# Optimization experiments

Hardware: AMD Instinct MI355X
Metric: run time of the kernel (lower is better)

## Reference

```python
import jax, jax.numpy as jnp
import numpy as np

B, T, D, H = 2, 2048, 1024, 16
HD = D // H            # head dim = 64
WINDOW = 512           # sliding-window size
EPS = 1e-6
ROPE_BASE = 10000.0


def setup_inputs() -> dict:
    key = jax.random.key(0)
    ks = jax.random.split(key, 5)
    s = 0.02  # init scale for dense kernels
    return {
        "x": jax.random.normal(ks[0], (B, T, D), jnp.float32),
        "Wq": jax.random.normal(ks[1], (D, D), jnp.float32) * s,
        "Wk": jax.random.normal(ks[2], (D, D), jnp.float32) * s,
        "Wv": jax.random.normal(ks[3], (D, D), jnp.float32) * s,
        "Wo": jax.random.normal(ks[4], (D, D), jnp.float32) * s,
        "q_scale": jnp.ones((HD,), jnp.float32),
        "k_scale": jnp.ones((HD,), jnp.float32),
        "sink_logit": jnp.zeros((H,), jnp.float32),
    }


def _rmsnorm(x, scale):
    # x: [..., HD]
    var = jnp.mean(jnp.square(x), axis=-1, keepdims=True)
    return x * jax.lax.rsqrt(var + EPS) * scale


def _rope(x):
    # x: [B, H, T, HD]; standard rotate-half RoPE over the full head dim
    half = HD // 2
    inv_freq = 1.0 / (ROPE_BASE ** (jnp.arange(0, HD, 2, dtype=jnp.float32) / HD))  # [half]
    t = jnp.arange(T, dtype=jnp.float32)
    freqs = t[:, None] * inv_freq[None, :]                # [T, half]
    emb = jnp.concatenate([freqs, freqs], axis=-1)        # [T, HD]
    cos = jnp.cos(emb)[None, None]                        # [1,1,T,HD]
    sin = jnp.sin(emb)[None, None]
    x1, x2 = x[..., :half], x[..., half:]
    rot = jnp.concatenate([-x2, x1], axis=-1)
    return x * cos + rot * sin


def reference(x, Wq, Wk, Wv, Wo, q_scale, k_scale, sink_logit):
    # projections -> [B, T, H, HD]
    q = (x @ Wq).reshape(B, T, H, HD)
    k = (x @ Wk).reshape(B, T, H, HD)
    v = (x @ Wv).reshape(B, T, H, HD)
    # QK RMSNorm over head dim
    q = _rmsnorm(q, q_scale)
    k = _rmsnorm(k, k_scale)
    # -> [B, H, T, HD], then RoPE
    q = _rope(q.transpose(0, 2, 1, 3))
    k = _rope(k.transpose(0, 2, 1, 3))
    v = v.transpose(0, 2, 1, 3)
    # causal sliding-window mask
    idx = jnp.arange(T)
    rel = idx[None, :] - idx[:, None]                     # key - query
    mask = ((rel <= 0) & (rel > -WINDOW))[None, None]     # [1,1,T,T]
    scale = HD ** (-0.5)
    scores = jnp.einsum('bhtd,bhsd->bhts', q, k) * scale
    scores = jnp.where(mask, scores, -jnp.inf)
    # sink-augmented softmax: append per-head sink logit to denominator
    sink = jnp.broadcast_to(sink_logit.reshape(1, H, 1, 1), (B, H, T, 1))
    aug = jnp.concatenate([scores.astype(jnp.float32), sink.astype(jnp.float32)], axis=-1)
    weights = jax.nn.softmax(aug, axis=-1)[..., :T].astype(scores.dtype)
    out = jnp.einsum('bhts,bhsd->bhtd', weights, v)
    out = out.transpose(0, 2, 1, 3).reshape(B, T, D)
    return out @ Wo
```

## Files before the change

### kernel.cpp

```cpp
#include <hip/hip_runtime.h>
#include <math.h>

#define CB 2
#define CT 2048
#define CD 1024
#define CH 16
#define CHD 64
#define CWINDOW 512

typedef __bf16 bf16x8 __attribute__((ext_vector_type(8)));
typedef float floatx4 __attribute__((ext_vector_type(4)));

__device__ __forceinline__ unsigned short f2bf(float f) {
  union { float f; unsigned int u; } v;
  v.f = f;
  unsigned int u = v.u;
  u += 0x7fffu + ((u >> 16) & 1u);
  return (unsigned short)(u >> 16);
}
__device__ __forceinline__ unsigned short f2bf_trunc(float f) {
  union { float f; unsigned int u; } v;
  v.f = f;
  return (unsigned short)(v.u >> 16);
}
__device__ __forceinline__ float bf2f(unsigned int h) {
  union { unsigned int u; float f; } v;
  v.u = h << 16;
  return v.f;
}

__global__ __launch_bounds__(256) void cvt_all(const float* __restrict__ x,
                                               const float* __restrict__ Wq,
                                               const float* __restrict__ Wk,
                                               const float* __restrict__ Wv,
                                               const float* __restrict__ Wo,
                                               unsigned short* __restrict__ xb,
                                               unsigned short* __restrict__ WqT,
                                               unsigned short* __restrict__ WkT,
                                               unsigned short* __restrict__ WvT,
                                               unsigned short* __restrict__ WoT) {
  const int z = blockIdx.z;
  if (z < 4) {
    const float* W = z == 0 ? Wq : z == 1 ? Wk : z == 2 ? Wv : Wo;
    unsigned short* Wt = z == 0 ? WqT : z == 1 ? WkT : z == 2 ? WvT : WoT;
    __shared__ float tile[64][65];
    const int k0 = blockIdx.x * 64, n0 = blockIdx.y * 64;
    const int c = threadIdx.x & 63, r4 = threadIdx.x >> 6;
#pragma unroll
    for (int i = 0; i < 16; ++i) {
      int r = i * 4 + r4;
      tile[r][c] = W[(size_t)(k0 + r) * CD + n0 + c];
    }
    __syncthreads();
#pragma unroll
    for (int i = 0; i < 16; ++i) {
      int r = i * 4 + r4;
      Wt[(size_t)(n0 + r) * CD + k0 + c] = f2bf(tile[c][r]);
    }
  } else {
    const int idx = (z - 4) * 256 + blockIdx.y * 16 + blockIdx.x;
    const int i = idx * 256 + threadIdx.x;
    float4 a = ((const float4*)x)[i * 2];
    float4 b = ((const float4*)x)[i * 2 + 1];
    uint4 o;
    o.x = (unsigned int)f2bf(a.x) | ((unsigned int)f2bf(a.y) << 16);
    o.y = (unsigned int)f2bf(a.z) | ((unsigned int)f2bf(a.w) << 16);
    o.z = (unsigned int)f2bf(b.x) | ((unsigned int)f2bf(b.y) << 16);
    o.w = (unsigned int)f2bf(b.z) | ((unsigned int)f2bf(b.w) << 16);
    ((uint4*)xb)[i] = o;
  }
}

__device__ __forceinline__ void async16(const unsigned short* g, unsigned short* l) {
  __builtin_amdgcn_global_load_lds(
      (const __attribute__((address_space(1))) unsigned int*)g,
      (__attribute__((address_space(3))) unsigned int*)l, 16, 0, 0);
}

__device__ __forceinline__ bf16x8 frag64(const unsigned short* base, int row, int ks, int lane) {
  const int phys = (((ks << 2) + (lane >> 4)) ^ (lane & 7)) << 3;
  return *(const bf16x8*)&base[(row << 6) + phys];
}

template <int MODE, int BM>
__device__ __forceinline__ void mfma_gemm_body(const unsigned short* __restrict__ A,
                                               const unsigned short* __restrict__ Bt,
                                               void* __restrict__ Cout,
                                               const float* __restrict__ scale,
                                               float oscale, int m0, int n0,
                                               unsigned short* __restrict__ As,
                                               unsigned short* __restrict__ Bs) {
  constexpr int K = CD;
  constexpr int MT = BM / 32;
  const int tid = threadIdx.x;
  const int wave = tid >> 6, lane = tid & 63;
  const int mq = (wave & 1) * (BM / 2), nq = (wave >> 1) * 64;

  floatx4 acc[MT][4] = {};
  const int l7 = lane & 7, l8 = lane >> 3;
  const int sxc = (l7 ^ l8) * 8;
  const int fr = lane & 15;

  for (int k0 = 0; k0 < K; k0 += 64) {
    __syncthreads();
#pragma unroll
    for (int it = 0; it < BM / 32; ++it) {
      const int s = wave * (BM / 32) + it;
      async16(A + (size_t)(m0 + s * 8 + l8) * K + k0 + sxc, &As[s * 512]);
    }
#pragma unroll
    for (int it = 0; it < 4; ++it) {
      const int s = wave * 4 + it;
      async16(Bt + (size_t)(n0 + s * 8 + l8) * K + k0 + sxc, &Bs[s * 512]);
    }
    __syncthreads();
#pragma unroll
    for (int ks = 0; ks < 2; ++ks) {
      bf16x8 af[MT], bg[4];
#pragma unroll
      for (int mt = 0; mt < MT; ++mt)
        af[mt] = frag64(As, mq + mt * 16 + fr, ks, lane);
#pragma unroll
      for (int nt = 0; nt < 4; ++nt)
        bg[nt] = frag64(Bs, nq + nt * 16 + fr, ks, lane);
#pragma unroll
      for (int mt = 0; mt < MT; ++mt)
#pragma unroll
        for (int nt = 0; nt < 4; ++nt)
          acc[mt][nt] = __builtin_amdgcn_mfma_f32_16x16x32_bf16(af[mt], bg[nt], acc[mt][nt], 0, 0, 0);
    }
  }

  if (MODE == 1) {
    const int c = lane & 15;
    const int g = lane >> 4;
    const int hh = (n0 + nq) >> 6;
    const float kf = -0.2878231366242557f;
    const float inv0 = __expf((float)c * kf);
    const float inv1 = __expf((float)(16 + c) * kf);
    float sc[4];
#pragma unroll
    for (int nt = 0; nt < 4; ++nt) sc[nt] = scale[nt * 16 + c];
#pragma unroll
    for (int mt = 0; mt < MT; ++mt) {
#pragma unroll
      for (int i = 0; i < 4; ++i) {
        const int m = m0 + mq + mt * 16 + g * 4 + i;
        const int b = m >> 11, t = m & (CT - 1);
        float v0 = acc[mt][0][i], v1 = acc[mt][1][i];
        float v2 = acc[mt][2][i], v3 = acc[mt][3][i];
        float ss = v0 * v0 + v1 * v1 + v2 * v2 + v3 * v3;
#pragma unroll
        for (int off = 8; off > 0; off >>= 1) ss += __shfl_xor(ss, off);
        const float rs = rsqrtf(ss * (1.0f / 64.0f) + 1e-6f);
        v0 *= rs * sc[0];
        v1 *= rs * sc[1];
        v2 *= rs * sc[2];
        v3 *= rs * sc[3];
        const float tf = (float)t;
        const float a0 = tf * inv0, a1 = tf * inv1;
        const float s0 = __sinf(a0), c0 = __cosf(a0);
        const float s1 = __sinf(a1), c1 = __cosf(a1);
        unsigned short* dst = (unsigned short*)Cout + ((size_t)(b * CH + hh) * CT + t) * CHD;
        ushort4 o;
        o.x = f2bf((v0 * c0 - v2 * s0) * oscale);
        o.y = f2bf((v1 * c1 - v3 * s1) * oscale);
        o.z = f2bf((v2 * c0 + v0 * s0) * oscale);
        o.w = f2bf((v3 * c1 + v1 * s1) * oscale);
        *(ushort4*)&dst[4 * c] = o;
      }
    }
  } else {
#pragma unroll
    for (int mt = 0; mt < MT; ++mt) {
#pragma unroll
      for (int nt = 0; nt < 4; ++nt) {
        const int col = n0 + nq + nt * 16 + (lane & 15);
        if (MODE == 2) {
          const int mb = m0 + mq + mt * 16 + (lane >> 4) * 4;
          const int b = mb >> 11, t = mb & (CT - 1);
          const int h = col >> 6, d = col & 63;
          ushort4 o;
          o.x = f2bf(acc[mt][nt][0]);
          o.y = f2bf(acc[mt][nt][1]);
          o.z = f2bf(acc[mt][nt][2]);
          o.w = f2bf(acc[mt][nt][3]);
          *(ushort4*)&((unsigned short*)Cout)[((size_t)(b * CH + h) * CHD + d) * CT + t] = o;
        } else {
#pragma unroll
          for (int i = 0; i < 4; ++i) {
            const int m = m0 + mq + mt * 16 + (lane >> 4) * 4 + i;
            ((float*)Cout)[(size_t)m * CD + col] = acc[mt][nt][i];
          }
        }
      }
    }
  }
}

__global__ __launch_bounds__(256, 3) void gemm_qkv_mfma(const unsigned short* __restrict__ xb,
                                                        const unsigned short* __restrict__ WqT,
                                                        const unsigned short* __restrict__ WkT,
                                                        const unsigned short* __restrict__ WvT,
                                                        unsigned short* __restrict__ Qh,
                                                        unsigned short* __restrict__ Kh,
                                                        unsigned short* __restrict__ Vt,
                                                        const float* __restrict__ q_scale,
                                                        const float* __restrict__ k_scale) {
  __shared__ unsigned short As[128 * 64];
  __shared__ unsigned short Bs[128 * 64];
  const unsigned int L = blockIdx.x + 32u * blockIdx.y + 256u * blockIdx.z;
  const unsigned int x = L & 7u;
  const unsigned int j = L >> 3;
  const unsigned int gm = x & 3u;
  const unsigned int gw = x >> 2;
  const unsigned int jm = j & 7u;
  const unsigned int jp = j >> 3;
  const int m0 = (int)(gm * 8u + jm) * 128;
  const unsigned int vp = gw * 12u + jp;
  const int n0 = (int)(vp & 7u) * 128;
  const int bz = (int)(vp >> 3);
  if (bz == 2) {
    mfma_gemm_body<2, 128>(xb, WvT, Vt, nullptr, 1.0f, m0, n0, As, Bs);
  } else if (bz == 0) {
    mfma_gemm_body<1, 128>(xb, WqT, Qh, q_scale, 0.125f, m0, n0, As, Bs);
  } else {
    mfma_gemm_body<1, 128>(xb, WkT, Kh, k_scale, 1.0f, m0, n0, As, Bs);
  }
}

__global__ __launch_bounds__(256, 3) void gemm_out_mfma(const unsigned short* __restrict__ AO,
                                                        const unsigned short* __restrict__ WoT,
                                                        float* __restrict__ out) {
  __shared__ unsigned short As[64 * 64];
  __shared__ unsigned short Bs[128 * 64];
  const unsigned int L = blockIdx.x + 64u * blockIdx.y;
  const unsigned int x = L & 7u;
  const unsigned int j = L >> 3;
  const unsigned int jm = j & 7u;
  const unsigned int jp = j >> 3;
  const int m0 = (int)(x * 8u + jm) * 64;
  const int n0 = (int)jp * 128;
  mfma_gemm_body<0, 64>(AO, WoT, out, nullptr, 1.0f, m0, n0, As, Bs);
}

__global__ __launch_bounds__(256, 2) void attn_mfma(const unsigned short* __restrict__ Qh,
                                                    const unsigned short* __restrict__ Kh,
                                                    const unsigned short* __restrict__ Vt,
                                                    const float* __restrict__ sink_logit,
                                                    unsigned short* __restrict__ AO) {
  __shared__ unsigned short Qs[128 * 64];
  __shared__ unsigned short Ks[2][64 * 64];
  __shared__ unsigned short Vs[2][64 * 64];
  __shared__ unsigned short Ps[128 * 72];

  const int tid = threadIdx.x;
  const int w = tid >> 6, lane = tid & 63;
  const unsigned int L = blockIdx.x + 16u * blockIdx.y;
  const int qb = (int)((L >> 3) & 15u);
  const int bh = (int)(L & 7u) * 4 + (int)(L >> 7);
  const int b = bh >> 4, h = bh & 15;
  const int q0 = qb * 128;
  const unsigned short* Qb = Qh + (size_t)bh * CT * CHD;
  const unsigned short* Kb = Kh + (size_t)bh * CT * CHD;
  const unsigned short* Vb = Vt + (size_t)bh * CHD * CT;

  const int l7 = lane & 7, l8 = lane >> 3;
  const int sx8 = (l7 ^ l8) * 8;

  const int kb_lo = (qb >= 4) ? (qb * 2 - 8) : 0;
  const int kb_hi = qb * 2 + 1;

#pragma unroll
  for (int s = 0; s < 4; ++s) {
    const int slab = w * 4 + s;
    async16(Qb + (size_t)(q0 + slab * 8 + l8) * CHD + sx8, &Qs[slab * 512]);
  }
#pragma unroll
  for (int s = 0; s < 2; ++s) {
    const int slab = w * 2 + s;
    const int row = slab * 8 + l8;
    async16(Kb + (size_t)(kb_lo * 64 + row) * CHD + sx8, &Ks[0][slab * 512]);
    async16(Vb + (size_t)row * CT + kb_lo * 64 + sx8, &Vs[0][slab * 512]);
  }
  __syncthreads();

  bf16x8 qf[2][2];
#pragma unroll
  for (int nt = 0; nt < 2; ++nt)
#pragma unroll
    for (int ks = 0; ks < 2; ++ks)
      qf[nt][ks] = frag64(Qs, w * 32 + nt * 16 + (lane & 15), ks, lane);

  bf16x8 vones;
#pragma unroll
  for (int i = 0; i < 8; ++i) vones[i] = (__bf16)1.0f;

  floatx4 acc[4][2] = {};
  floatx4 lsacc[2] = {};
  const int qw = q0 + w * 32;

  int cur = 0;
  for (int kb = kb_lo; kb <= kb_hi; ++kb) {
    if (kb < kb_hi) {
#pragma unroll
      for (int s = 0; s < 2; ++s) {
        const int slab = w * 2 + s;
        const int row = slab * 8 + l8;
        async16(Kb + (size_t)((kb + 1) * 64 + row) * CHD + sx8, &Ks[cur ^ 1][slab * 512]);
        async16(Vb + (size_t)row * CT + (kb + 1) * 64 + sx8, &Vs[cur ^ 1][slab * 512]);
      }
    }

    const int kmin = kb * 64, kmax = kb * 64 + 63;
    if (!(kmin > qw + 31 || kmax <= qw - CWINDOW)) {
      const unsigned short* Kc = Ks[cur];
      const unsigned short* Vc = Vs[cur];

      floatx4 st[4][2] = {};
#pragma unroll
      for (int ks = 0; ks < 2; ++ks) {
        bf16x8 kf[4];
#pragma unroll
        for (int mt = 0; mt < 4; ++mt)
          kf[mt] = frag64(Kc, mt * 16 + (lane & 15), ks, lane);
        __builtin_amdgcn_s_setprio(1);
#pragma unroll
        for (int mt = 0; mt < 4; ++mt)
#pragma unroll
          for (int nt = 0; nt < 2; ++nt)
            st[mt][nt] = __builtin_amdgcn_mfma_f32_16x16x32_bf16(kf[mt], qf[nt][ks], st[mt][nt], 0, 0, 0);
        __builtin_amdgcn_s_setprio(0);
      }

      const bool need_c = (kmax > qw);
      const bool need_w = (kmin <= qw + 31 - CWINDOW);
#pragma unroll
      for (int mt = 0; mt < 4; ++mt) {
#pragma unroll
        for (int nt = 0; nt < 2; ++nt) {
          const int s_base = kb * 64 + mt * 16 + (lane >> 4) * 4;
          const int t_g = q0 + w * 32 + nt * 16 + (lane & 15);
          ushort4 pk;
#pragma unroll
          for (int i = 0; i < 4; ++i) {
            float sv = st[mt][nt][i];
            if (need_c || need_w) {
              const int s_g = s_base + i;
              const bool ok = (!need_c || (s_g <= t_g)) && (!need_w || (s_g > t_g - CWINDOW));
              sv = ok ? sv : -INFINITY;
            }
            ((unsigned short*)&pk)[i] = f2bf_trunc(__expf(sv));
          }
          const int qrow = w * 32 + nt * 16 + (lane & 15);
          const int scol = mt * 16 + (lane >> 4) * 4;
          *(ushort4*)&Ps[qrow * 72 + scol] = pk;
        }
      }

#pragma unroll
      for (int ks = 0; ks < 2; ++ks) {
        bf16x8 vf[4], pf[2];
#pragma unroll
        for (int mt = 0; mt < 4; ++mt)
          vf[mt] = frag64(Vc, mt * 16 + (lane & 15), ks, lane);
#pragma unroll
        for (int nt = 0; nt < 2; ++nt) {
          const int qrow = w * 32 + nt * 16 + (lane & 15);
          pf[nt] = *(const bf16x8*)&Ps[qrow * 72 + ks * 32 + (lane >> 4) * 8];
        }
        __builtin_amdgcn_s_setprio(1);
#pragma unroll
        for (int mt = 0; mt < 4; ++mt)
#pragma unroll
          for (int nt = 0; nt < 2; ++nt)
            acc[mt][nt] = __builtin_amdgcn_mfma_f32_16x16x32_bf16(vf[mt], pf[nt], acc[mt][nt], 0, 0, 0);
#pragma unroll
        for (int nt = 0; nt < 2; ++nt)
          lsacc[nt] = __builtin_amdgcn_mfma_f32_16x16x32_bf16(vones, pf[nt], lsacc[nt], 0, 0, 0);
        __builtin_amdgcn_s_setprio(0);
      }
    }

    asm volatile("s_waitcnt vmcnt(0)" ::: "memory");
    __builtin_amdgcn_s_barrier();
    cur ^= 1;
  }

  const float sinkw = __expf(sink_logit[h]);
  float inv[2];
#pragma unroll
  for (int nt = 0; nt < 2; ++nt) inv[nt] = 1.0f / (lsacc[nt][0] + sinkw);
#pragma unroll
  for (int mt = 0; mt < 4; ++mt) {
#pragma unroll
    for (int nt = 0; nt < 2; ++nt) {
      const int t_g = q0 + w * 32 + nt * 16 + (lane & 15);
      const int d0 = mt * 16 + (lane >> 4) * 4;
      ushort4 o;
      o.x = f2bf(acc[mt][nt][0] * inv[nt]);
      o.y = f2bf(acc[mt][nt][1] * inv[nt]);
      o.z = f2bf(acc[mt][nt][2] * inv[nt]);
      o.w = f2bf(acc[mt][nt][3] * inv[nt]);
      *(ushort4*)&AO[(size_t)(b * CT + t_g) * CD + h * CHD + d0] = o;
    }
  }
}

extern "C" void kernel_launch(void* const* d_in, const int* in_sizes, int n_in,
                              void* d_out, int out_size, void* d_ws, size_t ws_size,
                              hipStream_t stream) {
  (void)in_sizes;
  (void)n_in;
  (void)out_size;
  (void)ws_size;
  const float* x = (const float*)d_in[0];
  const float* Wq = (const float*)d_in[1];
  const float* Wk = (const float*)d_in[2];
  const float* Wv = (const float*)d_in[3];
  const float* Wo = (const float*)d_in[4];
  const float* q_scale = (const float*)d_in[5];
  const float* k_scale = (const float*)d_in[6];
  const float* sink = (const float*)d_in[7];
  float* out = (float*)d_out;

  const size_t per = (size_t)CB * CH * CT * CHD;
  unsigned short* Qh = (unsigned short*)d_ws;
  unsigned short* Kh = Qh + per;
  unsigned short* Vt = Kh + per;
  unsigned short* AO = Vt + per;
  unsigned short* xb = AO + per;
  unsigned short* WqT = xb + per;
  unsigned short* WkT = WqT + (size_t)CD * CD;
  unsigned short* WvT = WkT + (size_t)CD * CD;
  unsigned short* WoT = WvT + (size_t)CD * CD;

  dim3 blk(256);
  cvt_all<<<dim3(16, 16, 12), blk, 0, stream>>>(x, Wq, Wk, Wv, Wo, xb, WqT, WkT, WvT, WoT);
  gemm_qkv_mfma<<<dim3(32, 8, 3), blk, 0, stream>>>(xb, WqT, WkT, WvT, Qh, Kh, Vt, q_scale, k_scale);
  attn_mfma<<<dim3(CT / 128, CB * CH), blk, 0, stream>>>(Qh, Kh, Vt, sink, AO);
  gemm_out_mfma<<<dim3(64, 8), blk, 0, stream>>>(AO, WoT, out);
}
```

Baseline: 156.6 us.

## Triple-buffer GEMM K-tiles with async LDS loads and a single barrier per step

```diff
diff --git a/kernel.cpp b/kernel.cpp
--- a/kernel.cpp
+++ b/kernel.cpp
@@ -77,9 +77,49 @@
       (__attribute__((address_space(3))) unsigned int*)l, 16, 0, 0);
 }
 
-__device__ __forceinline__ bf16x8 frag64(const unsigned short* base, int row, int ks, int lane) {
-  const int phys = (((ks << 2) + (lane >> 4)) ^ (lane & 7)) << 3;
-  return *(const bf16x8*)&base[(row << 6) + phys];
+__device__ __forceinline__ bf16x8 frag32(const unsigned short* base, int row, int lane) {
+  const int phys = ((lane >> 4) ^ (row & 3)) << 3;
+  return *(const bf16x8*)&base[(row << 5) + phys];
+}
+
+template <int BM>
+__device__ __forceinline__ void gemm_stage(const unsigned short* __restrict__ A,
+                                           const unsigned short* __restrict__ Bt,
+                                           unsigned short* __restrict__ As_s,
+                                           unsigned short* __restrict__ Bs_s,
+                                           int m0, int n0, int t, int wave, int lane) {
+  const int row_in = lane >> 2;
+  const int src_c = ((lane & 3) ^ (row_in & 3)) * 8;
+  const int k0 = t * 32;
+#pragma unroll
+  for (int it = 0; it < BM / 64; ++it) {
+    const int sub = wave * (BM / 64) + it;
+    async16(A + (size_t)(m0 + sub * 16 + row_in) * CD + k0 + src_c, &As_s[sub * 512]);
+  }
+#pragma unroll
+  for (int it = 0; it < 2; ++it) {
+    const int sub = wave * 2 + it;
+    async16(Bt + (size_t)(n0 + sub * 16 + row_in) * CD + k0 + src_c, &Bs_s[sub * 512]);
+  }
+}
+
+template <int MT>
+__device__ __forceinline__ void gemm_compute(const unsigned short* __restrict__ As_s,
+                                             const unsigned short* __restrict__ Bs_s,
+                                             floatx4 (&acc)[MT][4], int mq, int nq, int lane) {
+  const int fr = lane & 15;
+  bf16x8 af[MT], bg[4];
+#pragma unroll
+  for (int mt = 0; mt < MT; ++mt) af[mt] = frag32(As_s, mq + mt * 16 + fr, lane);
+#pragma unroll
+  for (int nt = 0; nt < 4; ++nt) bg[nt] = frag32(Bs_s, nq + nt * 16 + fr, lane);
+  __builtin_amdgcn_s_setprio(1);
+#pragma unroll
+  for (int mt = 0; mt < MT; ++mt)
+#pragma unroll
+    for (int nt = 0; nt < 4; ++nt)
+      acc[mt][nt] = __builtin_amdgcn_mfma_f32_16x16x32_bf16(af[mt], bg[nt], acc[mt][nt], 0, 0, 0);
+  __builtin_amdgcn_s_setprio(0);
 }
 
 template <int MODE, int BM>
@@ -90,46 +130,39 @@
                                                float oscale, int m0, int n0,
                                                unsigned short* __restrict__ As,
                                                unsigned short* __restrict__ Bs) {
-  constexpr int K = CD;
+  constexpr int NT = CD / 32;
   constexpr int MT = BM / 32;
+  constexpr int ASLOT = BM * 32;
+  constexpr int BSLOT = 128 * 32;
   const int tid = threadIdx.x;
   const int wave = tid >> 6, lane = tid & 63;
   const int mq = (wave & 1) * (BM / 2), nq = (wave >> 1) * 64;
 
   floatx4 acc[MT][4] = {};
-  const int l7 = lane & 7, l8 = lane >> 3;
-  const int sxc = (l7 ^ l8) * 8;
-  const int fr = lane & 15;
-
-  for (int k0 = 0; k0 < K; k0 += 64) {
-    __syncthreads();
-#pragma unroll
-    for (int it = 0; it < BM / 32; ++it) {
-      const int s = wave * (BM / 32) + it;
-      async16(A + (size_t)(m0 + s * 8 + l8) * K + k0 + sxc, &As[s * 512]);
-    }
-#pragma unroll
-    for (int it = 0; it < 4; ++it) {
-      const int s = wave * 4 + it;
-      async16(Bt + (size_t)(n0 + s * 8 + l8) * K + k0 + sxc, &Bs[s * 512]);
-    }
-    __syncthreads();
-#pragma unroll
-    for (int ks = 0; ks < 2; ++ks) {
-      bf16x8 af[MT], bg[4];
-#pragma unroll
-      for (int mt = 0; mt < MT; ++mt)
-        af[mt] = frag64(As, mq + mt * 16 + fr, ks, lane);
-#pragma unroll
-      for (int nt = 0; nt < 4; ++nt)
-        bg[nt] = frag64(Bs, nq + nt * 16 + fr, ks, lane);
-#pragma unroll
-      for (int mt = 0; mt < MT; ++mt)
-#pragma unroll
-        for (int nt = 0; nt < 4; ++nt)
-          acc[mt][nt] = __builtin_amdgcn_mfma_f32_16x16x32_bf16(af[mt], bg[nt], acc[mt][nt], 0, 0, 0);
-    }
-  }
+
+  gemm_stage<BM>(A, Bt, As, Bs, m0, n0, 0, wave, lane);
+  gemm_stage<BM>(A, Bt, As + ASLOT, Bs + BSLOT, m0, n0, 1, wave, lane);
+  if constexpr (BM == 128) asm volatile("s_waitcnt vmcnt(4)" ::: "memory");
+  else asm volatile("s_waitcnt vmcnt(3)" ::: "memory");
+  __builtin_amdgcn_s_barrier();
+
+#pragma unroll 1
+  for (int j = 0; j < (NT - 2) / 3; ++j) {
+#pragma unroll
+    for (int u = 0; u < 3; ++u) {
+      const int t = j * 3 + u;
+      const int ss = (u + 2) % 3;
+      gemm_stage<BM>(A, Bt, As + ss * ASLOT, Bs + ss * BSLOT, m0, n0, t + 2, wave, lane);
+      gemm_compute<MT>(As + u * ASLOT, Bs + u * BSLOT, acc, mq, nq, lane);
+      if constexpr (BM == 128) asm volatile("s_waitcnt vmcnt(4)" ::: "memory");
+      else asm volatile("s_waitcnt vmcnt(3)" ::: "memory");
+      __builtin_amdgcn_s_barrier();
+    }
+  }
+  gemm_compute<MT>(As + 0 * ASLOT, Bs + 0 * BSLOT, acc, mq, nq, lane);
+  asm volatile("s_waitcnt vmcnt(0)" ::: "memory");
+  __builtin_amdgcn_s_barrier();
+  gemm_compute<MT>(As + 1 * ASLOT, Bs + 1 * BSLOT, acc, mq, nq, lane);
 
   if (MODE == 1) {
     const int c = lane & 15;
@@ -207,8 +240,8 @@
                                                         unsigned short* __restrict__ Vt,
                                                         const float* __restrict__ q_scale,
                                                         const float* __restrict__ k_scale) {
-  __shared__ unsigned short As[128 * 64];
-  __shared__ unsigned short Bs[128 * 64];
+  __shared__ unsigned short As[3 * 128 * 32];
+  __shared__ unsigned short Bs[3 * 128 * 32];
   const unsigned int L = blockIdx.x + 32u * blockIdx.y + 256u * blockIdx.z;
   const unsigned int x = L & 7u;
   const unsigned int j = L >> 3;
@@ -232,8 +265,8 @@
 __global__ __launch_bounds__(256, 3) void gemm_out_mfma(const unsigned short* __restrict__ AO,
                                                         const unsigned short* __restrict__ WoT,
                                                         float* __restrict__ out) {
-  __shared__ unsigned short As[64 * 64];
-  __shared__ unsigned short Bs[128 * 64];
+  __shared__ unsigned short As[3 * 64 * 32];
+  __shared__ unsigned short Bs[3 * 128 * 32];
   const unsigned int L = blockIdx.x + 64u * blockIdx.y;
   const unsigned int x = L & 7u;
   const unsigned int j = L >> 3;
@@ -242,6 +275,11 @@
   const int m0 = (int)(x * 8u + jm) * 64;
   const int n0 = (int)jp * 128;
   mfma_gemm_body<0, 64>(AO, WoT, out, nullptr, 1.0f, m0, n0, As, Bs);
+}
+
+__device__ __forceinline__ bf16x8 frag64(const unsigned short* base, int row, int ks, int lane) {
+  const int phys = (((ks << 2) + (lane >> 4)) ^ (lane & 7)) << 3;
+  return *(const bf16x8*)&base[(row << 6) + phys];
 }
 
 __global__ __launch_bounds__(256, 2) void attn_mfma(const unsigned short* __restrict__ Qh,
```

Result: slower. 165.5 us (+5.6%).
